# Kernel optimization log

Measured on AMD Instinct MI355X. Metric: run time of the kernel, lower is better.

Reference implementation:

```python
import jax, jax.numpy as jnp
import numpy as np

N_NODES = 8192
HIDDEN = 256
OUT_DIM = 16
AVG_DEG = 32


def setup_inputs() -> dict:
    key = jax.random.key(0)
    ka, k1, k2, k3 = jax.random.split(key, 4)
    # Sparse symmetric binary adjacency, avg degree ~AVG_DEG, zero diagonal.
    p = AVG_DEG / (2.0 * N_NODES)  # symmetrization doubles density
    a = jax.random.uniform(ka, (N_NODES, N_NODES)) < p
    adj = jnp.logical_or(a, a.T).astype(jnp.float32)
    adj = adj * (1.0 - jnp.eye(N_NODES, dtype=jnp.float32))
    # Glorot-ish init for the GCN linear layers and the readout FC.
    W1 = jax.random.normal(k1, (1, HIDDEN), jnp.float32) * (2.0 / (1 + HIDDEN)) ** 0.5
    W2 = jax.random.normal(k2, (HIDDEN, HIDDEN), jnp.float32) * (2.0 / (2 * HIDDEN)) ** 0.5
    Wfc = jax.random.normal(k3, (HIDDEN, OUT_DIM), jnp.float32) * (2.0 / (HIDDEN + OUT_DIM)) ** 0.5
    return {
        "adj_matrix": adj,
        "W1": W1, "b1": jnp.zeros((HIDDEN,), jnp.float32),
        "W2": W2, "b2": jnp.zeros((HIDDEN,), jnp.float32),
        "Wfc": Wfc, "bfc": jnp.zeros((OUT_DIM,), jnp.float32),
    }


def _gcn_norm(adj_matrix):
    """Symmetrically normalized adjacency with self loops: D^-1/2 (A+I) D^-1/2."""
    n = adj_matrix.shape[0]
    A = (adj_matrix > 0).astype(adj_matrix.dtype)
    idx = jnp.arange(n)
    A = A.at[idx, idx].set(1.0)  # add_remaining_self_loops
    deg = A.sum(axis=1)
    dinv = jnp.where(deg > 0, jax.lax.rsqrt(deg), 0.0)
    return dinv[:, None] * A * dinv[None, :]


def reference(adj_matrix, W1, b1, W2, b2, Wfc, bfc):
    n = adj_matrix.shape[0]
    Nmat = _gcn_norm(adj_matrix)                       # [n, n]
    x = jnp.ones((n, 1), dtype=adj_matrix.dtype)       # node features = ones
    # GCNConv: aggregate(normed adj, x @ W) + bias
    h = jax.nn.relu(Nmat @ (x @ W1) + b1)              # [n, H]
    h = jax.nn.relu(Nmat @ (h @ W2) + b2)              # [n, H]
    pooled = h.sum(axis=0, keepdims=True)              # global_add_pool -> [1, H]
    return pooled @ Wfc + bfc                          # [1, OUT_DIM]
```

## Files before the change

kernel.cpp:

```cpp
#include <hip/hip_runtime.h>

#define N_NODES 8192
#define HIDDEN 256
#define OUT_DIM 16
#define CAP 128
#define G_ROWS 16
#define PBLK 512
#define NPB (N_NODES / PBLK)

__global__ void k_init(const float* __restrict__ W1, const float* __restrict__ b1,
                       const float* __restrict__ W2, int* __restrict__ cnt,
                       float* __restrict__ v, int* __restrict__ flag) {
    const int t = threadIdx.x;
    const int bid = blockIdx.x;
    if (bid < 32) {
        cnt[bid * 256 + t] = 0;
        return;
    }
    float acc = 0.0f;
    for (int k = 0; k < HIDDEN; ++k)
        acc += fmaxf(W1[k], 0.0f) * W2[(size_t)k * HIDDEN + t];
    v[t] = acc;
    __shared__ int nz;
    if (t == 0) nz = 0;
    __syncthreads();
    if (b1[t] != 0.0f) atomicOr(&nz, 1);
    __syncthreads();
    if (t == 0) *flag = (nz == 0) ? 1 : 0;
}

__device__ __forceinline__ void add_edge(int i, int j, int* cnt, int* nbr) {
    int p = atomicAdd(&cnt[i], 1);
    if (p < CAP) nbr[(size_t)i * CAP + p] = j;
    int q = atomicAdd(&cnt[j], 1);
    if (q < CAP) nbr[(size_t)j * CAP + q] = i;
}

__device__ __forceinline__ void scan_row(const float* __restrict__ adj, int i,
                                         int t, int* cnt, int* nbr) {
    const uint4* row4 = (const uint4*)(adj + (size_t)i * N_NODES);
    const int k0 = (i + 1) >> 2;
    for (int k = k0 + t; k < N_NODES / 4; k += 256) {
        uint4 vv = row4[k];
        if (vv.x | vv.y | vv.z | vv.w) {
            int base = k * 4;
            if (vv.x && base + 0 > i) add_edge(i, base + 0, cnt, nbr);
            if (vv.y && base + 1 > i) add_edge(i, base + 1, cnt, nbr);
            if (vv.z && base + 2 > i) add_edge(i, base + 2, cnt, nbr);
            if (vv.w && base + 3 > i) add_edge(i, base + 3, cnt, nbr);
        }
    }
}

__global__ void k_scan(const float* __restrict__ adj, int* __restrict__ cnt,
                       int* __restrict__ nbr) {
    const int t = threadIdx.x;
    const int ia = blockIdx.x;
    const int ib = N_NODES - 1 - ia;
    scan_row(adj, ia, t, cnt, nbr);
    scan_row(adj, ib, t, cnt, nbr);
}

__global__ void k_srow(const int* __restrict__ cnt, const int* __restrict__ nbr,
                       float* __restrict__ s, float* __restrict__ tt,
                       float* __restrict__ dinv) {
    const int w = threadIdx.x >> 6;
    const int lane = threadIdx.x & 63;
    const int i = blockIdx.x * 4 + w;
    const int c0 = cnt[i];
    const int c = c0 < CAP ? c0 : CAP;
    const float di = rsqrtf((float)(c0 + 1));
    float p = 0.0f;
    for (int k = lane; k < c; k += 64)
        p += rsqrtf((float)(cnt[nbr[(size_t)i * CAP + k]] + 1));
    #pragma unroll
    for (int off = 32; off > 0; off >>= 1) p += __shfl_down(p, off);
    if (lane == 0) {
        const float si = di * (di + p);
        s[i] = si; tt[i] = di * si; dinv[i] = di;
    }
}

__global__ void k_gemm(const float* __restrict__ s, const float* __restrict__ W1,
                       const float* __restrict__ b1, const float* __restrict__ W2,
                       const int* __restrict__ flag, float* __restrict__ g) {
    if (*flag) return;
    const int t = threadIdx.x;
    const int row0 = blockIdx.x * G_ROWS;
    __shared__ float hT[HIDDEN][G_ROWS];
    const float w1 = W1[t];
    const float bb = b1[t];
    for (int r = 0; r < G_ROWS; ++r)
        hT[t][r] = fmaxf(s[row0 + r] * w1 + bb, 0.0f);
    __syncthreads();

    float acc[G_ROWS];
    #pragma unroll
    for (int r = 0; r < G_ROWS; ++r) acc[r] = 0.0f;
    for (int k = 0; k < HIDDEN; ++k) {
        const float w2 = W2[(size_t)k * HIDDEN + t];
        const float4 h0 = *(const float4*)&hT[k][0];
        const float4 h1 = *(const float4*)&hT[k][4];
        const float4 h2 = *(const float4*)&hT[k][8];
        const float4 h3 = *(const float4*)&hT[k][12];
        acc[0]  += h0.x * w2;  acc[1]  += h0.y * w2;  acc[2]  += h0.z * w2;  acc[3]  += h0.w * w2;
        acc[4]  += h1.x * w2;  acc[5]  += h1.y * w2;  acc[6]  += h1.z * w2;  acc[7]  += h1.w * w2;
        acc[8]  += h2.x * w2;  acc[9]  += h2.y * w2;  acc[10] += h2.z * w2;  acc[11] += h2.w * w2;
        acc[12] += h3.x * w2;  acc[13] += h3.y * w2;  acc[14] += h3.z * w2;  acc[15] += h3.w * w2;
    }
    #pragma unroll
    for (int r = 0; r < G_ROWS; ++r)
        g[(size_t)(row0 + r) * HIDDEN + t] = acc[r];
}

__global__ void k_pool(const int* __restrict__ cnt, const int* __restrict__ nbr,
                       const float* __restrict__ s, const float* __restrict__ tt,
                       const float* __restrict__ dinv, const float* __restrict__ g,
                       const float* __restrict__ v, const float* __restrict__ b2,
                       const int* __restrict__ flag, float* __restrict__ P) {
    const int t = threadIdx.x;
    const int bid = blockIdx.x;
    if (*flag) {
        __shared__ float qsh[NPB];
        const int w = t >> 6, lane = t & 63;
        #pragma unroll
        for (int n = 0; n < NPB / 4; ++n) {
            const int i = bid * NPB + w * (NPB / 4) + n;
            const int c0 = cnt[i];
            const int c = c0 < CAP ? c0 : CAP;
            const float di = rsqrtf((float)(c0 + 1));
            float p = 0.0f;
            for (int k = lane; k < c; k += 64) p += tt[nbr[(size_t)i * CAP + k]];
            #pragma unroll
            for (int off = 32; off > 0; off >>= 1) p += __shfl_down(p, off);
            if (lane == 0) qsh[w * (NPB / 4) + n] = di * (di * s[i] + p);
        }
        __syncthreads();
        const float vc = v[t], bc = b2[t];
        float pp = 0.0f;
        #pragma unroll
        for (int n = 0; n < NPB; ++n) pp += fmaxf(qsh[n] * vc + bc, 0.0f);
        P[(size_t)bid * HIDDEN + t] = pp;
    } else {
        const float bb2 = b2[t];
        float pool = 0.0f;
        for (int n = 0; n < NPB; ++n) {
            const int i = bid * NPB + n;
            const float di = dinv[i];
            float val = di * g[(size_t)i * HIDDEN + t];
            const int c0 = cnt[i];
            const int c = c0 < CAP ? c0 : CAP;
            const int* nb = nbr + (size_t)i * CAP;
            for (int k = 0; k < c; ++k) {
                const int j = nb[k];
                val += dinv[j] * g[(size_t)j * HIDDEN + t];
            }
            val *= di;
            pool += fmaxf(val + bb2, 0.0f);
        }
        P[(size_t)bid * HIDDEN + t] = pool;
    }
}

__global__ void k_finish(const float* __restrict__ P, const float* __restrict__ Wfc,
                         const float* __restrict__ bfc, float* __restrict__ out) {
    const int t = threadIdx.x;
    float a0 = 0.f, a1 = 0.f, a2 = 0.f, a3 = 0.f;
    #pragma unroll 8
    for (int r = 0; r < PBLK; r += 4) {
        a0 += P[(size_t)(r + 0) * HIDDEN + t];
        a1 += P[(size_t)(r + 1) * HIDDEN + t];
        a2 += P[(size_t)(r + 2) * HIDDEN + t];
        a3 += P[(size_t)(r + 3) * HIDDEN + t];
    }
    __shared__ float pooled[HIDDEN];
    pooled[t] = (a0 + a1) + (a2 + a3);
    __syncthreads();
    const int o = t & 15, kg = t >> 4;
    float pr = 0.0f;
    for (int k = kg; k < HIDDEN; k += 16) pr += pooled[k] * Wfc[k * OUT_DIM + o];
    __shared__ float red[256];
    red[t] = pr;
    __syncthreads();
    if (t < OUT_DIM) {
        float sum = bfc[t];
        #pragma unroll
        for (int gg = 0; gg < 16; ++gg) sum += red[gg * 16 + t];
        out[t] = sum;
    }
}

extern "C" void kernel_launch(void* const* d_in, const int* in_sizes, int n_in,
                              void* d_out, int out_size, void* d_ws, size_t ws_size,
                              hipStream_t stream) {
    const float* adj = (const float*)d_in[0];
    const float* W1  = (const float*)d_in[1];
    const float* b1  = (const float*)d_in[2];
    const float* W2  = (const float*)d_in[3];
    const float* b2  = (const float*)d_in[4];
    const float* Wfc = (const float*)d_in[5];
    const float* bfc = (const float*)d_in[6];
    float* out = (float*)d_out;

    char* ws = (char*)d_ws;
    int*   cnt  = (int*)  (ws + 0);
    float* s    = (float*)(ws + (32 << 10));
    float* tt   = (float*)(ws + (64 << 10));
    float* dinv = (float*)(ws + (96 << 10));
    float* v    = (float*)(ws + (128 << 10));
    int*   flag = (int*)  (ws + (132 << 10));
    float* P    = (float*)(ws + (256 << 10));
    int*   nbr  = (int*)  (ws + (2 << 20));
    float* g    = (float*)(ws + (8 << 20));

    k_init  <<<33, 256, 0, stream>>>(W1, b1, W2, cnt, v, flag);
    k_scan  <<<N_NODES / 2, 256, 0, stream>>>(adj, cnt, nbr);
    k_srow  <<<N_NODES / 4, 256, 0, stream>>>(cnt, nbr, s, tt, dinv);
    k_gemm  <<<N_NODES / G_ROWS, 256, 0, stream>>>(s, W1, b1, W2, flag, g);
    k_pool  <<<PBLK, 256, 0, stream>>>(cnt, nbr, s, tt, dinv, g, v, b2, flag, P);
    k_finish<<<1, 256, 0, stream>>>(P, Wfc, bfc, out);
}
```

Baseline: 80.79 us.

## Replace per-node neighbor lists with compact edge list and scatter passes

```diff
diff --git a/kernel.cpp b/kernel.cpp
--- a/kernel.cpp
+++ b/kernel.cpp
@@ -3,18 +3,22 @@
 #define N_NODES 8192
 #define HIDDEN 256
 #define OUT_DIM 16
-#define CAP 128
-#define G_ROWS 16
 #define PBLK 512
 #define NPB (N_NODES / PBLK)
+#define ELDS 512
+#define EMAXG (1 << 20)
+#define G_ROWS 16
 
 __global__ void k_init(const float* __restrict__ W1, const float* __restrict__ b1,
-                       const float* __restrict__ W2, int* __restrict__ cnt,
-                       float* __restrict__ v, int* __restrict__ flag) {
+                       const float* __restrict__ W2, int* __restrict__ deg,
+                       float* __restrict__ sacc, float* __restrict__ qacc,
+                       int* __restrict__ ecnt, float* __restrict__ v,
+                       int* __restrict__ flag) {
     const int t = threadIdx.x;
     const int bid = blockIdx.x;
     if (bid < 32) {
-        cnt[bid * 256 + t] = 0;
+        const int idx = bid * 256 + t;
+        deg[idx] = 0; sacc[idx] = 0.0f; qacc[idx] = 0.0f;
         return;
     }
     float acc = 0.0f;
@@ -22,78 +26,111 @@
         acc += fmaxf(W1[k], 0.0f) * W2[(size_t)k * HIDDEN + t];
     v[t] = acc;
     __shared__ int nz;
-    if (t == 0) nz = 0;
+    if (t == 0) { nz = 0; *ecnt = 0; }
     __syncthreads();
     if (b1[t] != 0.0f) atomicOr(&nz, 1);
     __syncthreads();
     if (t == 0) *flag = (nz == 0) ? 1 : 0;
 }
 
-__device__ __forceinline__ void add_edge(int i, int j, int* cnt, int* nbr) {
-    int p = atomicAdd(&cnt[i], 1);
-    if (p < CAP) nbr[(size_t)i * CAP + p] = j;
-    int q = atomicAdd(&cnt[j], 1);
-    if (q < CAP) nbr[(size_t)j * CAP + q] = i;
-}
-
-__device__ __forceinline__ void scan_row(const float* __restrict__ adj, int i,
-                                         int t, int* cnt, int* nbr) {
+__device__ __forceinline__ void scan_row_tri(const float* __restrict__ adj, int i,
+                                             int t, int* ecl, int* el) {
     const uint4* row4 = (const uint4*)(adj + (size_t)i * N_NODES);
     const int k0 = (i + 1) >> 2;
     for (int k = k0 + t; k < N_NODES / 4; k += 256) {
         uint4 vv = row4[k];
         if (vv.x | vv.y | vv.z | vv.w) {
             int base = k * 4;
-            if (vv.x && base + 0 > i) add_edge(i, base + 0, cnt, nbr);
-            if (vv.y && base + 1 > i) add_edge(i, base + 1, cnt, nbr);
-            if (vv.z && base + 2 > i) add_edge(i, base + 2, cnt, nbr);
-            if (vv.w && base + 3 > i) add_edge(i, base + 3, cnt, nbr);
+            if (vv.x && base + 0 > i) { int p = atomicAdd(ecl, 1); if (p < ELDS) el[p] = (i << 13) | (base + 0); }
+            if (vv.y && base + 1 > i) { int p = atomicAdd(ecl, 1); if (p < ELDS) el[p] = (i << 13) | (base + 1); }
+            if (vv.z && base + 2 > i) { int p = atomicAdd(ecl, 1); if (p < ELDS) el[p] = (i << 13) | (base + 2); }
+            if (vv.w && base + 3 > i) { int p = atomicAdd(ecl, 1); if (p < ELDS) el[p] = (i << 13) | (base + 3); }
         }
     }
 }
 
-__global__ void k_scan(const float* __restrict__ adj, int* __restrict__ cnt,
-                       int* __restrict__ nbr) {
+__global__ void k_scan(const float* __restrict__ adj, int* __restrict__ ecnt,
+                       int* __restrict__ elist) {
     const int t = threadIdx.x;
     const int ia = blockIdx.x;
     const int ib = N_NODES - 1 - ia;
-    scan_row(adj, ia, t, cnt, nbr);
-    scan_row(adj, ib, t, cnt, nbr);
-}
-
-__global__ void k_srow(const int* __restrict__ cnt, const int* __restrict__ nbr,
-                       float* __restrict__ s, float* __restrict__ tt,
-                       float* __restrict__ dinv) {
-    const int w = threadIdx.x >> 6;
-    const int lane = threadIdx.x & 63;
-    const int i = blockIdx.x * 4 + w;
-    const int c0 = cnt[i];
-    const int c = c0 < CAP ? c0 : CAP;
-    const float di = rsqrtf((float)(c0 + 1));
-    float p = 0.0f;
-    for (int k = lane; k < c; k += 64)
-        p += rsqrtf((float)(cnt[nbr[(size_t)i * CAP + k]] + 1));
-    #pragma unroll
-    for (int off = 32; off > 0; off >>= 1) p += __shfl_down(p, off);
-    if (lane == 0) {
-        const float si = di * (di + p);
-        s[i] = si; tt[i] = di * si; dinv[i] = di;
-    }
-}
-
-__global__ void k_gemm(const float* __restrict__ s, const float* __restrict__ W1,
-                       const float* __restrict__ b1, const float* __restrict__ W2,
-                       const int* __restrict__ flag, float* __restrict__ g) {
+    __shared__ int ecl;
+    __shared__ int el[ELDS];
+    __shared__ int base_s;
+    if (t == 0) ecl = 0;
+    __syncthreads();
+    scan_row_tri(adj, ia, t, &ecl, el);
+    scan_row_tri(adj, ib, t, &ecl, el);
+    __syncthreads();
+    int n = ecl; if (n > ELDS) n = ELDS;
+    if (t == 0) base_s = atomicAdd(ecnt, n);
+    __syncthreads();
+    const int base = base_s;
+    for (int e = t; e < n; e += 256) {
+        const int idx = base + e;
+        if (idx < EMAXG) elist[idx] = el[e];
+    }
+}
+
+__global__ void k_deg(const int* __restrict__ ecnt, const int* __restrict__ elist,
+                      int* __restrict__ deg) {
+    int ne = *ecnt; if (ne > EMAXG) ne = EMAXG;
+    const int stride = gridDim.x * blockDim.x;
+    for (int e = blockIdx.x * blockDim.x + threadIdx.x; e < ne; e += stride) {
+        const int u = elist[e];
+        atomicAdd(&deg[u >> 13], 1);
+        atomicAdd(&deg[u & (N_NODES - 1)], 1);
+    }
+}
+
+__global__ void k_sscat(const int* __restrict__ ecnt, const int* __restrict__ elist,
+                        const int* __restrict__ deg, float* __restrict__ sacc) {
+    int ne = *ecnt; if (ne > EMAXG) ne = EMAXG;
+    const int stride = gridDim.x * blockDim.x;
+    for (int e = blockIdx.x * blockDim.x + threadIdx.x; e < ne; e += stride) {
+        const int u = elist[e];
+        const int i = u >> 13, j = u & (N_NODES - 1);
+        const float di = rsqrtf((float)(deg[i] + 1));
+        const float dj = rsqrtf((float)(deg[j] + 1));
+        atomicAdd(&sacc[i], dj);
+        atomicAdd(&sacc[j], di);
+    }
+}
+
+__global__ void k_qscat(const int* __restrict__ ecnt, const int* __restrict__ elist,
+                        const int* __restrict__ deg, const float* __restrict__ sacc,
+                        float* __restrict__ qacc) {
+    int ne = *ecnt; if (ne > EMAXG) ne = EMAXG;
+    const int stride = gridDim.x * blockDim.x;
+    for (int e = blockIdx.x * blockDim.x + threadIdx.x; e < ne; e += stride) {
+        const int u = elist[e];
+        const int i = u >> 13, j = u & (N_NODES - 1);
+        const float di = rsqrtf((float)(deg[i] + 1));
+        const float dj = rsqrtf((float)(deg[j] + 1));
+        const float tti = di * di * (di + sacc[i]);
+        const float ttj = dj * dj * (dj + sacc[j]);
+        atomicAdd(&qacc[i], ttj);
+        atomicAdd(&qacc[j], tti);
+    }
+}
+
+__global__ void k_gemm(const int* __restrict__ deg, const float* __restrict__ sacc,
+                       const float* __restrict__ W1, const float* __restrict__ b1,
+                       const float* __restrict__ W2, const int* __restrict__ flag,
+                       float* __restrict__ g) {
     if (*flag) return;
     const int t = threadIdx.x;
     const int row0 = blockIdx.x * G_ROWS;
     __shared__ float hT[HIDDEN][G_ROWS];
     const float w1 = W1[t];
     const float bb = b1[t];
-    for (int r = 0; r < G_ROWS; ++r)
-        hT[t][r] = fmaxf(s[row0 + r] * w1 + bb, 0.0f);
-    __syncthreads();
-
+    for (int r = 0; r < G_ROWS; ++r) {
+        const int i = row0 + r;
+        const float di = rsqrtf((float)(deg[i] + 1));
+        const float si = di * (di + sacc[i]);
+        hT[t][r] = fmaxf(si * w1 + bb, 0.0f);
+    }
+    __syncthreads();
     float acc[G_ROWS];
     #pragma unroll
     for (int r = 0; r < G_ROWS; ++r) acc[r] = 0.0f;
@@ -113,27 +150,20 @@
         g[(size_t)(row0 + r) * HIDDEN + t] = acc[r];
 }
 
-__global__ void k_pool(const int* __restrict__ cnt, const int* __restrict__ nbr,
-                       const float* __restrict__ s, const float* __restrict__ tt,
-                       const float* __restrict__ dinv, const float* __restrict__ g,
-                       const float* __restrict__ v, const float* __restrict__ b2,
-                       const int* __restrict__ flag, float* __restrict__ P) {
+__global__ void k_pool(const float* __restrict__ adj, const int* __restrict__ deg,
+                       const float* __restrict__ sacc, const float* __restrict__ qacc,
+                       const float* __restrict__ g, const float* __restrict__ v,
+                       const float* __restrict__ b2, const int* __restrict__ flag,
+                       float* __restrict__ P) {
     const int t = threadIdx.x;
     const int bid = blockIdx.x;
     if (*flag) {
         __shared__ float qsh[NPB];
-        const int w = t >> 6, lane = t & 63;
-        #pragma unroll
-        for (int n = 0; n < NPB / 4; ++n) {
-            const int i = bid * NPB + w * (NPB / 4) + n;
-            const int c0 = cnt[i];
-            const int c = c0 < CAP ? c0 : CAP;
-            const float di = rsqrtf((float)(c0 + 1));
-            float p = 0.0f;
-            for (int k = lane; k < c; k += 64) p += tt[nbr[(size_t)i * CAP + k]];
-            #pragma unroll
-            for (int off = 32; off > 0; off >>= 1) p += __shfl_down(p, off);
-            if (lane == 0) qsh[w * (NPB / 4) + n] = di * (di * s[i] + p);
+        if (t < NPB) {
+            const int i = bid * NPB + t;
+            const float di = rsqrtf((float)(deg[i] + 1));
+            const float si = di * (di + sacc[i]);
+            qsh[t] = di * (di * si + qacc[i]);
         }
         __syncthreads();
         const float vc = v[t], bc = b2[t];
@@ -142,21 +172,35 @@
         for (int n = 0; n < NPB; ++n) pp += fmaxf(qsh[n] * vc + bc, 0.0f);
         P[(size_t)bid * HIDDEN + t] = pp;
     } else {
-        const float bb2 = b2[t];
+        __shared__ int hl[ELDS];
+        __shared__ int hcnt;
+        const float bc = b2[t];
         float pool = 0.0f;
         for (int n = 0; n < NPB; ++n) {
             const int i = bid * NPB + n;
-            const float di = dinv[i];
-            float val = di * g[(size_t)i * HIDDEN + t];
-            const int c0 = cnt[i];
-            const int c = c0 < CAP ? c0 : CAP;
-            const int* nb = nbr + (size_t)i * CAP;
-            for (int k = 0; k < c; ++k) {
-                const int j = nb[k];
-                val += dinv[j] * g[(size_t)j * HIDDEN + t];
+            if (t == 0) hcnt = 0;
+            __syncthreads();
+            const uint4* row4 = (const uint4*)(adj + (size_t)i * N_NODES);
+            for (int k = t; k < N_NODES / 4; k += 256) {
+                uint4 vv = row4[k];
+                if (vv.x | vv.y | vv.z | vv.w) {
+                    int base = k * 4;
+                    if (vv.x && base + 0 != i) { int p = atomicAdd(&hcnt, 1); if (p < ELDS) hl[p] = base + 0; }
+                    if (vv.y && base + 1 != i) { int p = atomicAdd(&hcnt, 1); if (p < ELDS) hl[p] = base + 1; }
+                    if (vv.z && base + 2 != i) { int p = atomicAdd(&hcnt, 1); if (p < ELDS) hl[p] = base + 2; }
+                    if (vv.w && base + 3 != i) { int p = atomicAdd(&hcnt, 1); if (p < ELDS) hl[p] = base + 3; }
+                }
             }
-            val *= di;
-            pool += fmaxf(val + bb2, 0.0f);
+            __syncthreads();
+            const float di = rsqrtf((float)(deg[i] + 1));
+            float acc = di * g[(size_t)i * HIDDEN + t];
+            int nh = hcnt; if (nh > ELDS) nh = ELDS;
+            for (int e = 0; e < nh; ++e) {
+                const int j = hl[e];
+                acc += rsqrtf((float)(deg[j] + 1)) * g[(size_t)j * HIDDEN + t];
+            }
+            pool += fmaxf(di * acc + bc, 0.0f);
+            __syncthreads();
         }
         P[(size_t)bid * HIDDEN + t] = pool;
     }
@@ -203,20 +247,22 @@
     float* out = (float*)d_out;
 
     char* ws = (char*)d_ws;
-    int*   cnt  = (int*)  (ws + 0);
-    float* s    = (float*)(ws + (32 << 10));
-    float* tt   = (float*)(ws + (64 << 10));
-    float* dinv = (float*)(ws + (96 << 10));
-    float* v    = (float*)(ws + (128 << 10));
-    int*   flag = (int*)  (ws + (132 << 10));
+    int*   deg  = (int*)  (ws + 0);
+    float* sacc = (float*)(ws + (32 << 10));
+    float* qacc = (float*)(ws + (64 << 10));
+    float* v    = (float*)(ws + (96 << 10));
+    int*   flag = (int*)  (ws + (100 << 10));
+    int*   ecnt = (int*)  (ws + (104 << 10));
     float* P    = (float*)(ws + (256 << 10));
-    int*   nbr  = (int*)  (ws + (2 << 20));
+    int*   elist= (int*)  (ws + (1 << 20));
     float* g    = (float*)(ws + (8 << 20));
 
-    k_init  <<<33, 256, 0, stream>>>(W1, b1, W2, cnt, v, flag);
-    k_scan  <<<N_NODES / 2, 256, 0, stream>>>(adj, cnt, nbr);
-    k_srow  <<<N_NODES / 4, 256, 0, stream>>>(cnt, nbr, s, tt, dinv);
-    k_gemm  <<<N_NODES / G_ROWS, 256, 0, stream>>>(s, W1, b1, W2, flag, g);
-    k_pool  <<<PBLK, 256, 0, stream>>>(cnt, nbr, s, tt, dinv, g, v, b2, flag, P);
+    k_init  <<<33, 256, 0, stream>>>(W1, b1, W2, deg, sacc, qacc, ecnt, v, flag);
+    k_scan  <<<N_NODES / 2, 256, 0, stream>>>(adj, ecnt, elist);
+    k_deg   <<<256, 256, 0, stream>>>(ecnt, elist, deg);
+    k_sscat <<<256, 256, 0, stream>>>(ecnt, elist, deg, sacc);
+    k_qscat <<<256, 256, 0, stream>>>(ecnt, elist, deg, sacc, qacc);
+    k_gemm  <<<N_NODES / G_ROWS, 256, 0, stream>>>(deg, sacc, W1, b1, W2, flag, g);
+    k_pool  <<<PBLK, 256, 0, stream>>>(adj, deg, sacc, qacc, g, v, b2, flag, P);
     k_finish<<<1, 256, 0, stream>>>(P, Wfc, bfc, out);
 }
```

Result: slower. 159.9 us (+97.9%).

## Scan full adjacency rows with shared-memory counters and fold init into scan

Applied to the files above, without the earlier changes.

```diff
diff --git a/kernel.cpp b/kernel.cpp
--- a/kernel.cpp
+++ b/kernel.cpp
@@ -5,71 +5,70 @@
 #define OUT_DIM 16
 #define CAP 128
 #define G_ROWS 16
-#define PBLK 512
-#define NPB (N_NODES / PBLK)
-
-__global__ void k_init(const float* __restrict__ W1, const float* __restrict__ b1,
-                       const float* __restrict__ W2, int* __restrict__ cnt,
+#define POOL_BLK 64
+#define NPPB (N_NODES / POOL_BLK)
+
+__global__ void k_scan(const float* __restrict__ adj, const float* __restrict__ W1,
+                       const float* __restrict__ b1, const float* __restrict__ W2,
+                       int* __restrict__ cnt, int* __restrict__ nbr,
                        float* __restrict__ v, int* __restrict__ flag) {
     const int t = threadIdx.x;
     const int bid = blockIdx.x;
-    if (bid < 32) {
-        cnt[bid * 256 + t] = 0;
+
+    if (bid >= N_NODES) {
+        const int bv = bid - N_NODES;
+        __shared__ float sm[256];
+        __shared__ int nz;
+        if (t == 0) nz = 0;
+        __syncthreads();
+        if (bv == 0 && b1[t] != 0.0f) atomicOr(&nz, 1);
+        const int kg = t >> 4, cl = t & 15;
+        const int c = bv * 16 + cl;
+        float partial = 0.0f;
+        for (int k = kg; k < HIDDEN; k += 16)
+            partial += fmaxf(W1[k], 0.0f) * W2[(size_t)k * HIDDEN + c];
+        sm[t] = partial;
+        __syncthreads();
+        if (bv == 0 && t == 0) *flag = (nz == 0) ? 1 : 0;
+        if (t < 16) {
+            float acc = 0.0f;
+            #pragma unroll
+            for (int gg = 0; gg < 16; ++gg) acc += sm[gg * 16 + t];
+            v[bv * 16 + t] = acc;
+        }
         return;
     }
-    float acc = 0.0f;
-    for (int k = 0; k < HIDDEN; ++k)
-        acc += fmaxf(W1[k], 0.0f) * W2[(size_t)k * HIDDEN + t];
-    v[t] = acc;
-    __shared__ int nz;
-    if (t == 0) nz = 0;
-    __syncthreads();
-    if (b1[t] != 0.0f) atomicOr(&nz, 1);
-    __syncthreads();
-    if (t == 0) *flag = (nz == 0) ? 1 : 0;
-}
-
-__device__ __forceinline__ void add_edge(int i, int j, int* cnt, int* nbr) {
-    int p = atomicAdd(&cnt[i], 1);
-    if (p < CAP) nbr[(size_t)i * CAP + p] = j;
-    int q = atomicAdd(&cnt[j], 1);
-    if (q < CAP) nbr[(size_t)j * CAP + q] = i;
-}
-
-__device__ __forceinline__ void scan_row(const float* __restrict__ adj, int i,
-                                         int t, int* cnt, int* nbr) {
-    const uint4* row4 = (const uint4*)(adj + (size_t)i * N_NODES);
-    const int k0 = (i + 1) >> 2;
-    for (int k = k0 + t; k < N_NODES / 4; k += 256) {
-        uint4 vv = row4[k];
+
+    const int i = bid;
+    __shared__ int scnt;
+    if (t == 0) scnt = 0;
+    __syncthreads();
+    const uint4* row = (const uint4*)(adj + (size_t)i * N_NODES);
+    #pragma unroll
+    for (int c8 = 0; c8 < N_NODES / 4 / 256; ++c8) {
+        uint4 vv = row[c8 * 256 + t];
+        int base = (c8 * 256 + t) * 4;
         if (vv.x | vv.y | vv.z | vv.w) {
-            int base = k * 4;
-            if (vv.x && base + 0 > i) add_edge(i, base + 0, cnt, nbr);
-            if (vv.y && base + 1 > i) add_edge(i, base + 1, cnt, nbr);
-            if (vv.z && base + 2 > i) add_edge(i, base + 2, cnt, nbr);
-            if (vv.w && base + 3 > i) add_edge(i, base + 3, cnt, nbr);
-        }
-    }
-}
-
-__global__ void k_scan(const float* __restrict__ adj, int* __restrict__ cnt,
-                       int* __restrict__ nbr) {
-    const int t = threadIdx.x;
-    const int ia = blockIdx.x;
-    const int ib = N_NODES - 1 - ia;
-    scan_row(adj, ia, t, cnt, nbr);
-    scan_row(adj, ib, t, cnt, nbr);
+            if (vv.x && base + 0 != i) { int p = atomicAdd(&scnt, 1); if (p < CAP) nbr[(size_t)i * CAP + p] = base + 0; }
+            if (vv.y && base + 1 != i) { int p = atomicAdd(&scnt, 1); if (p < CAP) nbr[(size_t)i * CAP + p] = base + 1; }
+            if (vv.z && base + 2 != i) { int p = atomicAdd(&scnt, 1); if (p < CAP) nbr[(size_t)i * CAP + p] = base + 2; }
+            if (vv.w && base + 3 != i) { int p = atomicAdd(&scnt, 1); if (p < CAP) nbr[(size_t)i * CAP + p] = base + 3; }
+        }
+    }
+    __syncthreads();
+    if (t == 0) {
+        int c = scnt < CAP ? scnt : CAP;
+        cnt[i] = c;
+    }
 }
 
 __global__ void k_srow(const int* __restrict__ cnt, const int* __restrict__ nbr,
-                       float* __restrict__ s, float* __restrict__ tt,
-                       float* __restrict__ dinv) {
+                       float* __restrict__ s, float* __restrict__ tt) {
     const int w = threadIdx.x >> 6;
     const int lane = threadIdx.x & 63;
     const int i = blockIdx.x * 4 + w;
-    const int c0 = cnt[i];
-    const int c = c0 < CAP ? c0 : CAP;
-    const float di = rsqrtf((float)(c0 + 1));
+    const int c = cnt[i];
+    const float di = rsqrtf((float)(c + 1));
     float p = 0.0f;
     for (int k = lane; k < c; k += 64)
         p += rsqrtf((float)(cnt[nbr[(size_t)i * CAP + k]] + 1));
@@ -77,7 +76,7 @@
     for (int off = 32; off > 0; off >>= 1) p += __shfl_down(p, off);
     if (lane == 0) {
         const float si = di * (di + p);
-        s[i] = si; tt[i] = di * si; dinv[i] = di;
+        s[i] = si; tt[i] = di * si;
     }
 }
 
@@ -93,7 +92,6 @@
     for (int r = 0; r < G_ROWS; ++r)
         hT[t][r] = fmaxf(s[row0 + r] * w1 + bb, 0.0f);
     __syncthreads();
-
     float acc[G_ROWS];
     #pragma unroll
     for (int r = 0; r < G_ROWS; ++r) acc[r] = 0.0f;
@@ -115,48 +113,44 @@
 
 __global__ void k_pool(const int* __restrict__ cnt, const int* __restrict__ nbr,
                        const float* __restrict__ s, const float* __restrict__ tt,
-                       const float* __restrict__ dinv, const float* __restrict__ g,
-                       const float* __restrict__ v, const float* __restrict__ b2,
-                       const int* __restrict__ flag, float* __restrict__ P) {
+                       const float* __restrict__ g, const float* __restrict__ v,
+                       const float* __restrict__ b2, const int* __restrict__ flag,
+                       float* __restrict__ P) {
     const int t = threadIdx.x;
     const int bid = blockIdx.x;
     if (*flag) {
-        __shared__ float qsh[NPB];
+        __shared__ float qsh[NPPB];
         const int w = t >> 6, lane = t & 63;
-        #pragma unroll
-        for (int n = 0; n < NPB / 4; ++n) {
-            const int i = bid * NPB + w * (NPB / 4) + n;
-            const int c0 = cnt[i];
-            const int c = c0 < CAP ? c0 : CAP;
-            const float di = rsqrtf((float)(c0 + 1));
+        for (int r = 0; r < NPPB / 4; ++r) {
+            const int i = bid * NPPB + r * 4 + w;
+            const int c = cnt[i];
+            const float di = rsqrtf((float)(c + 1));
             float p = 0.0f;
             for (int k = lane; k < c; k += 64) p += tt[nbr[(size_t)i * CAP + k]];
             #pragma unroll
             for (int off = 32; off > 0; off >>= 1) p += __shfl_down(p, off);
-            if (lane == 0) qsh[w * (NPB / 4) + n] = di * (di * s[i] + p);
+            if (lane == 0) qsh[r * 4 + w] = di * (di * s[i] + p);
         }
         __syncthreads();
         const float vc = v[t], bc = b2[t];
         float pp = 0.0f;
-        #pragma unroll
-        for (int n = 0; n < NPB; ++n) pp += fmaxf(qsh[n] * vc + bc, 0.0f);
+        #pragma unroll 8
+        for (int n = 0; n < NPPB; ++n) pp += fmaxf(qsh[n] * vc + bc, 0.0f);
         P[(size_t)bid * HIDDEN + t] = pp;
     } else {
-        const float bb2 = b2[t];
+        const float bc = b2[t];
         float pool = 0.0f;
-        for (int n = 0; n < NPB; ++n) {
-            const int i = bid * NPB + n;
-            const float di = dinv[i];
+        for (int n = 0; n < NPPB; ++n) {
+            const int i = bid * NPPB + n;
+            const int c = cnt[i];
+            const float di = rsqrtf((float)(c + 1));
             float val = di * g[(size_t)i * HIDDEN + t];
-            const int c0 = cnt[i];
-            const int c = c0 < CAP ? c0 : CAP;
             const int* nb = nbr + (size_t)i * CAP;
             for (int k = 0; k < c; ++k) {
                 const int j = nb[k];
-                val += dinv[j] * g[(size_t)j * HIDDEN + t];
+                val += rsqrtf((float)(cnt[j] + 1)) * g[(size_t)j * HIDDEN + t];
             }
-            val *= di;
-            pool += fmaxf(val + bb2, 0.0f);
+            pool += fmaxf(di * val + bc, 0.0f);
         }
         P[(size_t)bid * HIDDEN + t] = pool;
     }
@@ -166,8 +160,8 @@
                          const float* __restrict__ bfc, float* __restrict__ out) {
     const int t = threadIdx.x;
     float a0 = 0.f, a1 = 0.f, a2 = 0.f, a3 = 0.f;
-    #pragma unroll 8
-    for (int r = 0; r < PBLK; r += 4) {
+    #pragma unroll
+    for (int r = 0; r < POOL_BLK; r += 4) {
         a0 += P[(size_t)(r + 0) * HIDDEN + t];
         a1 += P[(size_t)(r + 1) * HIDDEN + t];
         a2 += P[(size_t)(r + 2) * HIDDEN + t];
@@ -206,17 +200,15 @@
     int*   cnt  = (int*)  (ws + 0);
     float* s    = (float*)(ws + (32 << 10));
     float* tt   = (float*)(ws + (64 << 10));
-    float* dinv = (float*)(ws + (96 << 10));
-    float* v    = (float*)(ws + (128 << 10));
-    int*   flag = (int*)  (ws + (132 << 10));
-    float* P    = (float*)(ws + (256 << 10));
-    int*   nbr  = (int*)  (ws + (2 << 20));
+    float* v    = (float*)(ws + (96 << 10));
+    int*   flag = (int*)  (ws + (100 << 10));
+    float* P    = (float*)(ws + (128 << 10));
+    int*   nbr  = (int*)  (ws + (1 << 20));
     float* g    = (float*)(ws + (8 << 20));
 
-    k_init  <<<33, 256, 0, stream>>>(W1, b1, W2, cnt, v, flag);
-    k_scan  <<<N_NODES / 2, 256, 0, stream>>>(adj, cnt, nbr);
-    k_srow  <<<N_NODES / 4, 256, 0, stream>>>(cnt, nbr, s, tt, dinv);
+    k_scan  <<<N_NODES + 16, 256, 0, stream>>>(adj, W1, b1, W2, cnt, nbr, v, flag);
+    k_srow  <<<N_NODES / 4, 256, 0, stream>>>(cnt, nbr, s, tt);
     k_gemm  <<<N_NODES / G_ROWS, 256, 0, stream>>>(s, W1, b1, W2, flag, g);
-    k_pool  <<<PBLK, 256, 0, stream>>>(cnt, nbr, s, tt, dinv, g, v, b2, flag, P);
+    k_pool  <<<POOL_BLK, 256, 0, stream>>>(cnt, nbr, s, tt, g, v, b2, flag, P);
     k_finish<<<1, 256, 0, stream>>>(P, Wfc, bfc, out);
 }
```

After: 86.41 us. +7.0%, slower.
